# Kernel optimization log

Hardware: AMD Instinct MI355X
Metric: run time of the kernel (lower is better)

Reference implementation:

```python
import jax, jax.numpy as jnp
import numpy as np

H = 1024   # hidden size
E = 8      # num experts
B, S = 4, 2048


def setup_inputs() -> dict:
    key = jax.random.key(0)
    k1, k2, k3, k4 = jax.random.split(key, 4)
    x = jax.random.normal(k1, (B, S, H), dtype=jnp.float32)
    wg = jax.random.normal(k2, (H, E), dtype=jnp.float32) * 0.02      # gate weight
    W = jax.random.normal(k3, (E, H, H), dtype=jnp.float32) * 0.02    # expert Linear weights (out, in) per expert
    b = jax.random.normal(k4, (E, H), dtype=jnp.float32) * 0.02       # expert Linear biases
    return {"x": x, "wg": wg, "W": W, "b": b}


def reference(x, wg, W, b):
    Bb, Ss, Hh = x.shape
    Ee = wg.shape[1]
    T = Bb * Ss
    C = T // Ee  # capacity (capacity_factor = 1.0, top-1)

    xt = x.reshape(T, Hh)
    logits = xt @ wg                                   # [T, E]
    probs = jax.nn.softmax(logits, axis=-1)            # [T, E]
    idx = jnp.argmax(probs, axis=-1)                   # [T] top-1 expert
    mask = jax.nn.one_hot(idx, Ee, dtype=xt.dtype)     # [T, E]

    # position of each token within its expert's queue (0-based)
    locations = jnp.cumsum(mask, axis=0) - mask        # [T, E]
    # drop tokens over capacity
    mask = mask * (locations < C).astype(xt.dtype)
    gate = jnp.sum(probs * mask, axis=-1)              # [T] gate prob (0 if dropped)
    loc_s = jnp.sum(locations * mask, axis=-1).astype(jnp.int32)  # [T]
    loc_oh = jax.nn.one_hot(loc_s, C, dtype=xt.dtype)  # [T, C]

    dispatch = mask[:, :, None] * loc_oh[:, None, :]   # [T, E, C]
    combine = gate[:, None, None] * dispatch           # [T, E, C]

    # dispatch tokens -> per-expert buffers [E, C, H]
    exp_in = jnp.einsum('tec,th->ech', dispatch, xt)
    # per-expert Linear: y = x @ W_e^T + b_e
    exp_out = jnp.einsum('ech,efh->ecf', exp_in, W) + b[:, None, :]
    # combine back to tokens, scaled by gate prob
    out = jnp.einsum('tec,ecf->tf', combine, exp_out)  # [T, H]
    return out.reshape(Bb, Ss, Hh)
```

## Files before the change

kernel.cpp:

```cpp
#include <hip/hip_runtime.h>

#define H 1024
#define E 8
#define T 8192
#define CAP 1024

typedef __bf16 bf16x8 __attribute__((ext_vector_type(8)));
typedef float  f32x4  __attribute__((ext_vector_type(4)));
typedef unsigned short u16;

__device__ __forceinline__ u16 f2bf(float f) {
    union { float f; unsigned u; } v; v.f = f;
    unsigned r = v.u + 0x7FFFu + ((v.u >> 16) & 1u);
    return (u16)(r >> 16);
}

typedef __attribute__((address_space(1))) const void* gas_t;
typedef __attribute__((address_space(3))) void* las_t;
__device__ __forceinline__ void gld16(const void* g, void* l) {
    __builtin_amdgcn_global_load_lds((gas_t)g, (las_t)l, 16, 0, 0);
}

__global__ __launch_bounds__(256) void wgt_kernel(
    const float* __restrict__ wg, float* __restrict__ wgT) {
    const int h = blockIdx.x * 256 + threadIdx.x;
    float4 lo = *(const float4*)(wg + h * E);
    float4 hi = *(const float4*)(wg + h * E + 4);
    wgT[0 * H + h] = lo.x; wgT[1 * H + h] = lo.y;
    wgT[2 * H + h] = lo.z; wgT[3 * H + h] = lo.w;
    wgT[4 * H + h] = hi.x; wgT[5 * H + h] = hi.y;
    wgT[6 * H + h] = hi.z; wgT[7 * H + h] = hi.w;
}

#define GATE_BLOCKS 512
#define CVT_BLOCKS  1536

__global__ __launch_bounds__(256) void gatecvt_kernel(
    const float* __restrict__ x, const float* __restrict__ wgT,
    const float* __restrict__ W,
    int* __restrict__ eid, float* __restrict__ gate,
    u16* __restrict__ xbf, u16* __restrict__ Wbf) {
    const int tid = threadIdx.x;

    if (blockIdx.x >= GATE_BLOCKS) {
        int i = (blockIdx.x - GATE_BLOCKS) * 256 + tid;
        const int n4 = E * H * H / 4;
        const int stride = CVT_BLOCKS * 256;
        for (; i < n4; i += stride) {
            float4 v = ((const float4*)W)[i];
            ushort4 o;
            o.x = f2bf(v.x); o.y = f2bf(v.y); o.z = f2bf(v.z); o.w = f2bf(v.w);
            ((ushort4*)Wbf)[i] = o;
        }
        return;
    }

    const int wv = tid >> 6, lane = tid & 63;
    const int tbase = blockIdx.x * 16 + wv * 4;
    const int h00 = lane * 4;

    float a[4][8];
    #pragma unroll
    for (int j = 0; j < 4; ++j)
        #pragma unroll
        for (int e = 0; e < 8; ++e) a[j][e] = 0.f;

    #pragma unroll
    for (int q = 0; q < 4; ++q) {
        const int h0 = q * 256 + h00;
        float4 xv[4];
        #pragma unroll
        for (int j = 0; j < 4; ++j)
            xv[j] = *(const float4*)(x + (size_t)(tbase + j) * H + h0);
        #pragma unroll
        for (int j = 0; j < 4; ++j) {
            ushort4 o;
            o.x = f2bf(xv[j].x); o.y = f2bf(xv[j].y);
            o.z = f2bf(xv[j].z); o.w = f2bf(xv[j].w);
            *(ushort4*)(xbf + (size_t)(tbase + j) * H + h0) = o;
        }
        #pragma unroll
        for (int e = 0; e < 8; ++e) {
            const float4 w4 = *(const float4*)(wgT + e * H + h0);
            #pragma unroll
            for (int j = 0; j < 4; ++j)
                a[j][e] += xv[j].x * w4.x + xv[j].y * w4.y
                         + xv[j].z * w4.z + xv[j].w * w4.w;
        }
    }

    const bool b0 = lane & 1, b1 = lane & 2, b2 = lane & 4;
    const int elane = ((lane & 1) << 2) | (lane & 2) | ((lane >> 2) & 1);

    #pragma unroll
    for (int j = 0; j < 4; ++j) {
        float* A = a[j];
        #pragma unroll
        for (int k = 0; k < 4; ++k) {
            float t = b0 ? A[k] : A[k + 4];
            t = __shfl_xor(t, 1);
            A[k] = (b0 ? A[k + 4] : A[k]) + t;
        }
        #pragma unroll
        for (int k = 0; k < 2; ++k) {
            float t = b1 ? A[k] : A[k + 2];
            t = __shfl_xor(t, 2);
            A[k] = (b1 ? A[k + 2] : A[k]) + t;
        }
        {
            float t = b2 ? A[0] : A[1];
            t = __shfl_xor(t, 4);
            A[0] = (b2 ? A[1] : A[0]) + t;
        }
        float v = A[0];
        v += __shfl_xor(v, 8); v += __shfl_xor(v, 16); v += __shfl_xor(v, 32);
        float m = v; int mi = elane;
        #pragma unroll
        for (int off = 1; off <= 4; off <<= 1) {
            float om = __shfl_xor(m, off);
            int   oi = __shfl_xor(mi, off);
            if (om > m || (om == m && oi < mi)) { m = om; mi = oi; }
        }
        float s = expf(v - m);
        s += __shfl_xor(s, 1); s += __shfl_xor(s, 2); s += __shfl_xor(s, 4);
        if (lane == 0) {
            eid[tbase + j]  = mi;
            gate[tbase + j] = 1.0f / s;
        }
    }
}

#define TPT 32
__global__ __launch_bounds__(256) void scan_kernel(
    const int* __restrict__ eid, float* __restrict__ gate,
    int* __restrict__ perm) {
    __shared__ int cnt[256][E];
    __shared__ int base[256][E];
    __shared__ int part[E][8];
    const int tid = threadIdx.x;

    for (int i = tid; i < E * CAP; i += 256) perm[i] = -1;

    const int t0 = tid * TPT;
    int c[E];
    #pragma unroll
    for (int e = 0; e < E; ++e) c[e] = 0;
    for (int i = 0; i < TPT; ++i) {
        const int ei = eid[t0 + i];
        #pragma unroll
        for (int e = 0; e < E; ++e) c[e] += (ei == e);
    }
    #pragma unroll
    for (int e = 0; e < E; ++e) cnt[tid][e] = c[e];
    __syncthreads();
    if (tid < 64) {
        const int e = tid >> 3, j = tid & 7;
        int s = 0;
        for (int i = j * 32; i < j * 32 + 32; ++i) s += cnt[i][e];
        part[e][j] = s;
    }
    __syncthreads();
    if (tid < E) {
        int run = 0;
        #pragma unroll
        for (int j = 0; j < 8; ++j) { int v = part[tid][j]; part[tid][j] = run; run += v; }
    }
    __syncthreads();
    if (tid < 64) {
        const int e = tid >> 3, j = tid & 7;
        int run = part[e][j];
        for (int i = j * 32; i < j * 32 + 32; ++i) { base[i][e] = run; run += cnt[i][e]; }
    }
    __syncthreads();
    #pragma unroll
    for (int e = 0; e < E; ++e) c[e] = base[tid][e];
    for (int i = 0; i < TPT; ++i) {
        const int t = t0 + i;
        const int ei = eid[t];
        int pos = 0;
        #pragma unroll
        for (int e = 0; e < E; ++e) if (ei == e) pos = c[e]++;
        if (pos < CAP) perm[ei * CAP + pos] = t;
        else gate[t] = 0.f;
    }
}

__global__ __launch_bounds__(256) void moe_gemm_bf(
    const u16* __restrict__ xbf, const u16* __restrict__ Wbf,
    const float* __restrict__ bias, const int* __restrict__ perm,
    const float* __restrict__ gate, float* __restrict__ out) {
    __shared__ __align__(16) u16 As[2][128 * 64];
    __shared__ __align__(16) u16 Bs[2][128 * 64];
    __shared__ int   perm_s[128];
    __shared__ float gate_s[128];

    const int tid = threadIdx.x;

    if (blockIdx.z == 8) {
        const int t = (blockIdx.y * 8 + blockIdx.x) * 128 + (tid >> 1);
        if (gate[t] == 0.f) {
            const int half = tid & 1;
            float4 z = make_float4(0.f, 0.f, 0.f, 0.f);
            float4* o = (float4*)(out + (size_t)t * H + half * 512);
            #pragma unroll
            for (int i = 0; i < 128; ++i) o[i] = z;
        }
        return;
    }

    const int e  = blockIdx.z;
    const int mb = blockIdx.y;
    const int fb = blockIdx.x;

    if (tid < 128) {
        const int t = perm[e * CAP + mb * 128 + tid];
        perm_s[tid] = t;
        gate_s[tid] = (t >= 0) ? gate[t] : 0.f;
    }
    __syncthreads();

    const int lane = tid & 63;
    const int wv = tid >> 6;
    const int wm = wv >> 1, wn = wv & 1;
    const int l16 = lane & 15, quad = lane >> 4;

    const int rl  = lane >> 3;
    const int cch = lane & 7;
    const int gch = cch ^ rl;
    const u16* ga[4]; const u16* gb[4];
    #pragma unroll
    for (int q = 0; q < 4; ++q) {
        const int r = (wv * 4 + q) * 8 + rl;
        const int tA = perm_s[r];
        const int tok = tA >= 0 ? tA : 0;
        ga[q] = xbf + (size_t)tok * H + gch * 8;
        gb[q] = Wbf + (size_t)e * H * H + (size_t)(fb * 128 + r) * H + gch * 8;
    }

    f32x4 acc[4][4] = {};

    for (int kt = 0; kt < H / 128; ++kt) {
        __syncthreads();
        #pragma unroll
        for (int hb = 0; hb < 2; ++hb)
            #pragma unroll
            for (int q = 0; q < 4; ++q) {
                gld16(ga[q] + hb * 64, &As[hb][(wv * 4 + q) * 512 + lane * 8]);
                gld16(gb[q] + hb * 64, &Bs[hb][(wv * 4 + q) * 512 + lane * 8]);
            }
        #pragma unroll
        for (int q = 0; q < 4; ++q) { ga[q] += 128; gb[q] += 128; }
        __syncthreads();
        #pragma unroll
        for (int hb = 0; hb < 2; ++hb)
            #pragma unroll
            for (int s = 0; s < 2; ++s) {
                bf16x8 af[4], bfr[4];
                const int cc = (s * 4 + quad) ^ (l16 & 7);
                #pragma unroll
                for (int i = 0; i < 4; ++i) {
                    af[i]  = *(const bf16x8*)&As[hb][(wm * 64 + i * 16 + l16) * 64 + cc * 8];
                    bfr[i] = *(const bf16x8*)&Bs[hb][(wn * 64 + i * 16 + l16) * 64 + cc * 8];
                }
                #pragma unroll
                for (int mi = 0; mi < 4; ++mi)
                    #pragma unroll
                    for (int ni = 0; ni < 4; ++ni)
                        acc[mi][ni] = __builtin_amdgcn_mfma_f32_16x16x32_bf16(
                            af[mi], bfr[ni], acc[mi][ni], 0, 0, 0);
            }
    }

    float bv[4];
    #pragma unroll
    for (int ni = 0; ni < 4; ++ni)
        bv[ni] = bias[e * H + fb * 128 + wn * 64 + ni * 16 + l16];

    #pragma unroll
    for (int mi = 0; mi < 4; ++mi) {
        #pragma unroll
        for (int r = 0; r < 4; ++r) {
            const int rowl = wm * 64 + mi * 16 + quad * 4 + r;
            const int t = perm_s[rowl];
            if (t < 0) continue;
            const float g = gate_s[rowl];
            float* orow = out + (size_t)t * H + fb * 128 + wn * 64;
            #pragma unroll
            for (int ni = 0; ni < 4; ++ni)
                orow[ni * 16 + l16] = g * (acc[mi][ni][r] + bv[ni]);
        }
    }
}

extern "C" void kernel_launch(void* const* d_in, const int* in_sizes, int n_in,
                              void* d_out, int out_size, void* d_ws, size_t ws_size,
                              hipStream_t stream) {
    const float* x    = (const float*)d_in[0];
    const float* wg   = (const float*)d_in[1];
    const float* W    = (const float*)d_in[2];
    const float* bias = (const float*)d_in[3];
    float* out = (float*)d_out;

    int*   eid  = (int*)d_ws;
    float* gate = (float*)((char*)d_ws + (size_t)T * 4);
    int*   perm = (int*)((char*)d_ws + (size_t)T * 8);
    float* wgT  = (float*)((char*)d_ws + (size_t)T * 12);
    u16*   xbf  = (u16*)((char*)d_ws + (size_t)T * 12 + (size_t)E * H * 4);
    u16*   Wbf  = xbf + (size_t)T * H;

    wgt_kernel<<<H / 256, 256, 0, stream>>>(wg, wgT);
    gatecvt_kernel<<<GATE_BLOCKS + CVT_BLOCKS, 256, 0, stream>>>(
        x, wgT, W, eid, gate, xbf, Wbf);
    scan_kernel<<<1, 256, 0, stream>>>(eid, gate, perm);
    moe_gemm_bf<<<dim3(8, 8, 9), 256, 0, stream>>>(xbf, Wbf, bias, perm, gate, out);
}
```

Before: 159.3 us.

## Use 512-thread blocks with 8 waves per 128x128 tile and expert-major block order

```diff
diff --git a/kernel.cpp b/kernel.cpp
--- a/kernel.cpp
+++ b/kernel.cpp
@@ -185,7 +185,7 @@
     }
 }
 
-__global__ __launch_bounds__(256) void moe_gemm_bf(
+__global__ __launch_bounds__(512, 4) void moe_gemm_bf(
     const u16* __restrict__ xbf, const u16* __restrict__ Wbf,
     const float* __restrict__ bias, const int* __restrict__ perm,
     const float* __restrict__ gate, float* __restrict__ out) {
@@ -195,22 +195,23 @@
     __shared__ float gate_s[128];
 
     const int tid = threadIdx.x;
-
-    if (blockIdx.z == 8) {
-        const int t = (blockIdx.y * 8 + blockIdx.x) * 128 + (tid >> 1);
+    const int idx = blockIdx.x;
+
+    if (idx >= 512) {
+        const int t = (idx - 512) * 128 + (tid >> 2);
         if (gate[t] == 0.f) {
-            const int half = tid & 1;
+            const int part = tid & 3;
             float4 z = make_float4(0.f, 0.f, 0.f, 0.f);
-            float4* o = (float4*)(out + (size_t)t * H + half * 512);
-            #pragma unroll
-            for (int i = 0; i < 128; ++i) o[i] = z;
+            float4* o = (float4*)(out + (size_t)t * H + part * 256);
+            #pragma unroll
+            for (int i = 0; i < 64; ++i) o[i] = z;
         }
         return;
     }
 
-    const int e  = blockIdx.z;
-    const int mb = blockIdx.y;
-    const int fb = blockIdx.x;
+    const int fb = idx >> 6;
+    const int mb = (idx >> 3) & 7;
+    const int e  = idx & 7;
 
     if (tid < 128) {
         const int t = perm[e * CAP + mb * 128 + tid];
@@ -221,60 +222,64 @@
 
     const int lane = tid & 63;
     const int wv = tid >> 6;
-    const int wm = wv >> 1, wn = wv & 1;
+    const int wm = wv >> 2;
+    const int wn = wv & 3;
     const int l16 = lane & 15, quad = lane >> 4;
 
     const int rl  = lane >> 3;
     const int cch = lane & 7;
     const int gch = cch ^ rl;
-    const u16* ga[4]; const u16* gb[4];
-    #pragma unroll
-    for (int q = 0; q < 4; ++q) {
-        const int r = (wv * 4 + q) * 8 + rl;
+    const u16* ga[2]; const u16* gb[2];
+    #pragma unroll
+    for (int q = 0; q < 2; ++q) {
+        const int r = wv * 16 + q * 8 + rl;
         const int tA = perm_s[r];
         const int tok = tA >= 0 ? tA : 0;
         ga[q] = xbf + (size_t)tok * H + gch * 8;
         gb[q] = Wbf + (size_t)e * H * H + (size_t)(fb * 128 + r) * H + gch * 8;
     }
 
-    f32x4 acc[4][4] = {};
+    f32x4 acc[4][2] = {};
 
     for (int kt = 0; kt < H / 128; ++kt) {
         __syncthreads();
         #pragma unroll
         for (int hb = 0; hb < 2; ++hb)
             #pragma unroll
-            for (int q = 0; q < 4; ++q) {
-                gld16(ga[q] + hb * 64, &As[hb][(wv * 4 + q) * 512 + lane * 8]);
-                gld16(gb[q] + hb * 64, &Bs[hb][(wv * 4 + q) * 512 + lane * 8]);
+            for (int q = 0; q < 2; ++q) {
+                u16* la = &As[hb][(wv * 16 + q * 8) * 64 + lane * 8];
+                u16* lb = &Bs[hb][(wv * 16 + q * 8) * 64 + lane * 8];
+                gld16(ga[q] + hb * 64, la);
+                gld16(gb[q] + hb * 64, lb);
             }
         #pragma unroll
-        for (int q = 0; q < 4; ++q) { ga[q] += 128; gb[q] += 128; }
+        for (int q = 0; q < 2; ++q) { ga[q] += 128; gb[q] += 128; }
         __syncthreads();
         #pragma unroll
         for (int hb = 0; hb < 2; ++hb)
             #pragma unroll
             for (int s = 0; s < 2; ++s) {
-                bf16x8 af[4], bfr[4];
+                bf16x8 af[4], bfr[2];
                 const int cc = (s * 4 + quad) ^ (l16 & 7);
                 #pragma unroll
-                for (int i = 0; i < 4; ++i) {
-                    af[i]  = *(const bf16x8*)&As[hb][(wm * 64 + i * 16 + l16) * 64 + cc * 8];
-                    bfr[i] = *(const bf16x8*)&Bs[hb][(wn * 64 + i * 16 + l16) * 64 + cc * 8];
-                }
+                for (int i = 0; i < 4; ++i)
+                    af[i] = *(const bf16x8*)&As[hb][(wm * 64 + i * 16 + l16) * 64 + cc * 8];
+                #pragma unroll
+                for (int i = 0; i < 2; ++i)
+                    bfr[i] = *(const bf16x8*)&Bs[hb][(wn * 32 + i * 16 + l16) * 64 + cc * 8];
                 #pragma unroll
                 for (int mi = 0; mi < 4; ++mi)
                     #pragma unroll
-                    for (int ni = 0; ni < 4; ++ni)
+                    for (int ni = 0; ni < 2; ++ni)
                         acc[mi][ni] = __builtin_amdgcn_mfma_f32_16x16x32_bf16(
                             af[mi], bfr[ni], acc[mi][ni], 0, 0, 0);
             }
     }
 
-    float bv[4];
-    #pragma unroll
-    for (int ni = 0; ni < 4; ++ni)
-        bv[ni] = bias[e * H + fb * 128 + wn * 64 + ni * 16 + l16];
+    float bv[2];
+    #pragma unroll
+    for (int ni = 0; ni < 2; ++ni)
+        bv[ni] = bias[e * H + fb * 128 + wn * 32 + ni * 16 + l16];
 
     #pragma unroll
     for (int mi = 0; mi < 4; ++mi) {
@@ -284,9 +289,9 @@
             const int t = perm_s[rowl];
             if (t < 0) continue;
             const float g = gate_s[rowl];
-            float* orow = out + (size_t)t * H + fb * 128 + wn * 64;
-            #pragma unroll
-            for (int ni = 0; ni < 4; ++ni)
+            float* orow = out + (size_t)t * H + fb * 128 + wn * 32;
+            #pragma unroll
+            for (int ni = 0; ni < 2; ++ni)
                 orow[ni * 16 + l16] = g * (acc[mi][ni][r] + bv[ni]);
         }
     }
@@ -312,5 +317,5 @@
     gatecvt_kernel<<<GATE_BLOCKS + CVT_BLOCKS, 256, 0, stream>>>(
         x, wgT, W, eid, gate, xbf, Wbf);
     scan_kernel<<<1, 256, 0, stream>>>(eid, gate, perm);
-    moe_gemm_bf<<<dim3(8, 8, 9), 256, 0, stream>>>(xbf, Wbf, bias, perm, gate, out);
-}
+    moe_gemm_bf<<<512 + 64, 512, 0, stream>>>(xbf, Wbf, bias, perm, gate, out);
+}
```

Result: faster. 153.4 us (-3.7%).
